# Kernel tuning notes

Measured on AMD Instinct MI355X. Metric: run time of the kernel, lower is better.

Reference implementation:

```python
import jax, jax.numpy as jnp
import numpy as np

B, N = 8192, 128
ALPHA, BETA = 0.5, 0.5
SIGMA1 = 0.01  # prior diagonal variance used in the temporal KL term


def setup_inputs() -> dict:
    key = jax.random.key(0)
    k1, k2, k3, k4, k5 = jax.random.split(key, 5)
    y = jax.random.normal(k1, (B, N), dtype=jnp.float32)
    mu = jax.random.normal(k2, (B, N), dtype=jnp.float32)
    lmbda = jax.random.uniform(k3, (B, N), dtype=jnp.float32, minval=0.5, maxval=2.0)
    psi = 0.1 * jax.random.normal(k4, (B, N, N), dtype=jnp.float32)
    # nu must be > n + 1 so the NIW variance is positive
    nu = jax.random.uniform(k5, (B, N), dtype=jnp.float32, minval=N + 2.0, maxval=N + 12.0)
    return {"y": y, "mu": mu, "lmbda": lmbda, "psi": psi, "nu": nu}


def reference(y, mu, lmbda, psi, nu):
    n = mu.shape[-1]
    y = jnp.nan_to_num(y, nan=0.0)

    # niw_var = diagonal(exp(psi) / (lmbda*(nu-n-1))[...,None]); only the
    # diagonal of psi contributes, so extract it first (same math, less traffic).
    psi_diag = jnp.diagonal(psi, axis1=-2, axis2=-1)              # [B, n]
    niw_var = jnp.exp(psi_diag) / (lmbda * (nu - n - 1.0))        # [B, n]

    # Multivariate KL between diag-Gaussians N(y, SIGMA1*I) and N(mu, diag(niw_var)),
    # with diagonal det/inverse/trace reduced to elementwise ops.
    mu_diff = mu - y
    term_1 = jnp.sum(jnp.log(niw_var), axis=-1) - n * jnp.log(jnp.asarray(SIGMA1, niw_var.dtype))
    term_2 = jnp.sum(SIGMA1 / niw_var, axis=-1)
    term_3 = jnp.sum(mu_diff * mu_diff / niw_var, axis=-1)
    kl = 0.5 * (term_1 - n + term_2 + term_3)                     # [B]
    temporal = jnp.sum(kl)                                        # 'sum' reduction -> scalar

    # L1 evidential error term
    evidence = lmbda + nu                                         # [B, n]
    error = jnp.mean(jnp.sum(jnp.abs(y - mu) * evidence, axis=-1))

    loss = ALPHA * temporal + BETA * error
    return loss, temporal, error
```

## Files before the change

kernel.cpp:

```cpp
#include <hip/hip_runtime.h>
#include <math.h>

#define BB 8192
#define NN 128

constexpr int BLOCK = 256;
constexpr int TOTAL_VEC = (BB * NN) / 4;
constexpr int GRID = TOTAL_VEC / BLOCK;

__global__ __launch_bounds__(BLOCK) void niw_reduce_kernel(
    const float* __restrict__ y, const float* __restrict__ mu,
    const float* __restrict__ lmbda, const float* __restrict__ psi,
    const float* __restrict__ nu, double* __restrict__ partials)
{
    const int v = blockIdx.x * BLOCK + threadIdx.x;
    const int e = v * 4;
    const int b = e >> 7;
    const int j = e & 127;

    const float4 yv  = *reinterpret_cast<const float4*>(y + e);
    const float4 muv = *reinterpret_cast<const float4*>(mu + e);
    const float4 lmv = *reinterpret_cast<const float4*>(lmbda + e);
    const float4 nuv = *reinterpret_cast<const float4*>(nu + e);

    const float* prow = psi + (size_t)b * (NN * NN) + (size_t)j * (NN + 1);
    float pd0 = prow[0];
    float pd1 = prow[129];
    float pd2 = prow[258];
    float pd3 = prow[387];

    const float yy[4] = {yv.x, yv.y, yv.z, yv.w};
    const float mm[4] = {muv.x, muv.y, muv.z, muv.w};
    const float ll[4] = {lmv.x, lmv.y, lmv.z, lmv.w};
    const float nn[4] = {nuv.x, nuv.y, nuv.z, nuv.w};
    const float pd[4] = {pd0, pd1, pd2, pd3};

    float s1 = 0.f, s2 = 0.f, s3 = 0.f, s4 = 0.f;
#pragma unroll
    for (int k = 0; k < 4; ++k) {
        float yk = yy[k];
        yk = (yk != yk) ? 0.0f : yk;
        const float d = mm[k] - yk;
        const float denom = ll[k] * (nn[k] - (float)(NN + 1));
        const float logv  = pd[k] - __logf(denom);
        const float inv_v = denom * __expf(-pd[k]);
        s1 += logv;
        s2 += inv_v;
        s3 += d * d * inv_v;
        s4 += fabsf(d) * (ll[k] + nn[k]);
    }

    double d1 = s1, d2 = s2, d3 = s3, d4 = s4;
#pragma unroll
    for (int off = 32; off > 0; off >>= 1) {
        d1 += __shfl_down(d1, off);
        d2 += __shfl_down(d2, off);
        d3 += __shfl_down(d3, off);
        d4 += __shfl_down(d4, off);
    }

    __shared__ double sh[4][4];
    const int wave = threadIdx.x >> 6;
    const int lane = threadIdx.x & 63;
    if (lane == 0) {
        sh[wave][0] = d1; sh[wave][1] = d2; sh[wave][2] = d3; sh[wave][3] = d4;
    }
    __syncthreads();
    if (threadIdx.x == 0) {
        double t1 = 0, t2 = 0, t3 = 0, t4 = 0;
        for (int w = 0; w < 4; ++w) {
            t1 += sh[w][0]; t2 += sh[w][1]; t3 += sh[w][2]; t4 += sh[w][3];
        }
        double* p = partials + (size_t)blockIdx.x * 4;
        p[0] = t1; p[1] = t2; p[2] = t3; p[3] = t4;
    }
}

__global__ __launch_bounds__(256) void niw_finalize_kernel(
    const double* __restrict__ partials, float* __restrict__ out)
{
    double t1 = 0, t2 = 0, t3 = 0, t4 = 0;
    for (int i = threadIdx.x; i < GRID; i += 256) {
        const double* p = partials + (size_t)i * 4;
        t1 += p[0]; t2 += p[1]; t3 += p[2]; t4 += p[3];
    }
#pragma unroll
    for (int off = 32; off > 0; off >>= 1) {
        t1 += __shfl_down(t1, off);
        t2 += __shfl_down(t2, off);
        t3 += __shfl_down(t3, off);
        t4 += __shfl_down(t4, off);
    }
    __shared__ double sh[4][4];
    const int wave = threadIdx.x >> 6;
    const int lane = threadIdx.x & 63;
    if (lane == 0) {
        sh[wave][0] = t1; sh[wave][1] = t2; sh[wave][2] = t3; sh[wave][3] = t4;
    }
    __syncthreads();
    if (threadIdx.x == 0) {
        double S1 = 0, S2 = 0, S3 = 0, S4 = 0;
        for (int w = 0; w < 4; ++w) {
            S1 += sh[w][0]; S2 += sh[w][1]; S3 += sh[w][2]; S4 += sh[w][3];
        }
        const double SIGMA1 = 0.01;
        const double n = (double)NN;
        const double Bd = (double)BB;
        const double temporal =
            0.5 * (S1 - Bd * n * log(SIGMA1) - Bd * n + SIGMA1 * S2 + S3);
        const double error = S4 / Bd;
        const double loss = 0.5 * temporal + 0.5 * error;
        out[0] = (float)loss;
        out[1] = (float)temporal;
        out[2] = (float)error;
    }
}

extern "C" void kernel_launch(void* const* d_in, const int* in_sizes, int n_in,
                              void* d_out, int out_size, void* d_ws, size_t ws_size,
                              hipStream_t stream) {
    const float* y     = (const float*)d_in[0];
    const float* mu    = (const float*)d_in[1];
    const float* lmbda = (const float*)d_in[2];
    const float* psi   = (const float*)d_in[3];
    const float* nu    = (const float*)d_in[4];
    float* out = (float*)d_out;
    double* partials = (double*)d_ws;

    niw_reduce_kernel<<<GRID, BLOCK, 0, stream>>>(y, mu, lmbda, psi, nu, partials);
    niw_finalize_kernel<<<1, 256, 0, stream>>>(partials, out);
}
```

Baseline: 30.36 us.

## Halve elements per thread, use nontemporal loads, reduce in float within waves

Each thread now handles 2 elements instead of 4, which doubles the grid and the number of independent psi diagonal gathers in flight. All input loads use nontemporal hints to avoid cache pollution from the streaming reads. The wave shuffle reduction and shared-memory staging switch from double to float, which cuts 64-bit shuffle cost but loses some accumulation precision. Block partials stay double for the finalize step.

```diff
diff --git a/kernel.cpp b/kernel.cpp
--- a/kernel.cpp
+++ b/kernel.cpp
@@ -4,66 +4,60 @@
 #define BB 8192
 #define NN 128
 
+typedef float vf2 __attribute__((ext_vector_type(2)));
+
 constexpr int BLOCK = 256;
-constexpr int TOTAL_VEC = (BB * NN) / 4;
-constexpr int GRID = TOTAL_VEC / BLOCK;
+constexpr int EPT = 2;
+constexpr int GRID = (BB * NN) / (BLOCK * EPT);
 
 __global__ __launch_bounds__(BLOCK) void niw_reduce_kernel(
     const float* __restrict__ y, const float* __restrict__ mu,
     const float* __restrict__ lmbda, const float* __restrict__ psi,
     const float* __restrict__ nu, double* __restrict__ partials)
 {
-    const int v = blockIdx.x * BLOCK + threadIdx.x;
-    const int e = v * 4;
+    const int t = blockIdx.x * BLOCK + threadIdx.x;
+    const int e = t * EPT;
     const int b = e >> 7;
     const int j = e & 127;
 
-    const float4 yv  = *reinterpret_cast<const float4*>(y + e);
-    const float4 muv = *reinterpret_cast<const float4*>(mu + e);
-    const float4 lmv = *reinterpret_cast<const float4*>(lmbda + e);
-    const float4 nuv = *reinterpret_cast<const float4*>(nu + e);
+    const float* prow = psi + (size_t)b * (NN * NN) + (size_t)j * (NN + 1);
+    const float pd0 = __builtin_nontemporal_load(prow);
+    const float pd1 = __builtin_nontemporal_load(prow + (NN + 1));
 
-    const float* prow = psi + (size_t)b * (NN * NN) + (size_t)j * (NN + 1);
-    float pd0 = prow[0];
-    float pd1 = prow[129];
-    float pd2 = prow[258];
-    float pd3 = prow[387];
+    const vf2 yv  = __builtin_nontemporal_load(reinterpret_cast<const vf2*>(y + e));
+    const vf2 muv = __builtin_nontemporal_load(reinterpret_cast<const vf2*>(mu + e));
+    const vf2 lmv = __builtin_nontemporal_load(reinterpret_cast<const vf2*>(lmbda + e));
+    const vf2 nuv = __builtin_nontemporal_load(reinterpret_cast<const vf2*>(nu + e));
 
-    const float yy[4] = {yv.x, yv.y, yv.z, yv.w};
-    const float mm[4] = {muv.x, muv.y, muv.z, muv.w};
-    const float ll[4] = {lmv.x, lmv.y, lmv.z, lmv.w};
-    const float nn[4] = {nuv.x, nuv.y, nuv.z, nuv.w};
-    const float pd[4] = {pd0, pd1, pd2, pd3};
+    const float pd[2] = {pd0, pd1};
 
     float s1 = 0.f, s2 = 0.f, s3 = 0.f, s4 = 0.f;
 #pragma unroll
-    for (int k = 0; k < 4; ++k) {
-        float yk = yy[k];
+    for (int k = 0; k < 2; ++k) {
+        float yk = yv[k];
         yk = (yk != yk) ? 0.0f : yk;
-        const float d = mm[k] - yk;
-        const float denom = ll[k] * (nn[k] - (float)(NN + 1));
-        const float logv  = pd[k] - __logf(denom);
+        const float d = muv[k] - yk;
+        const float denom = lmv[k] * (nuv[k] - (float)(NN + 1));
+        s1 += pd[k] - __logf(denom);
         const float inv_v = denom * __expf(-pd[k]);
-        s1 += logv;
         s2 += inv_v;
         s3 += d * d * inv_v;
-        s4 += fabsf(d) * (ll[k] + nn[k]);
+        s4 += fabsf(d) * (lmv[k] + nuv[k]);
     }
 
-    double d1 = s1, d2 = s2, d3 = s3, d4 = s4;
 #pragma unroll
     for (int off = 32; off > 0; off >>= 1) {
-        d1 += __shfl_down(d1, off);
-        d2 += __shfl_down(d2, off);
-        d3 += __shfl_down(d3, off);
-        d4 += __shfl_down(d4, off);
+        s1 += __shfl_down(s1, off);
+        s2 += __shfl_down(s2, off);
+        s3 += __shfl_down(s3, off);
+        s4 += __shfl_down(s4, off);
     }
 
-    __shared__ double sh[4][4];
+    __shared__ float sh[4][4];
     const int wave = threadIdx.x >> 6;
     const int lane = threadIdx.x & 63;
     if (lane == 0) {
-        sh[wave][0] = d1; sh[wave][1] = d2; sh[wave][2] = d3; sh[wave][3] = d4;
+        sh[wave][0] = s1; sh[wave][1] = s2; sh[wave][2] = s3; sh[wave][3] = s4;
     }
     __syncthreads();
     if (threadIdx.x == 0) {
```

Measured after the change: 31.58 us. 4.0% more time.
